# Kernel optimization log

Hardware: AMD Instinct MI355X
Metric: run time of the kernel (lower is better)

## Reference

```python
import jax, jax.numpy as jnp
import numpy as np
import math

PHI = (1 + math.sqrt(5)) / 2
COMPRESS_EXP = 2.0 / 3.0
ALPHA_D = 0.01


def c_mag(z):
    return jnp.sqrt(z[..., 0] ** 2 + z[..., 1] ** 2 + 1e-08)


def c_phase(z):
    return jnp.arctan2(z[..., 1], z[..., 0] + 1e-10)


def c_mul(a, b):
    real = a[..., 0] * b[..., 0] - a[..., 1] * b[..., 1]
    imag = a[..., 0] * b[..., 1] + a[..., 1] * b[..., 0]
    return jnp.stack([real, imag], axis=-1)


@jax.custom_vjp
def fractal_compress(mag):
    return jnp.clip(mag, 1e-08) ** COMPRESS_EXP


def _fc_fwd(mag):
    ms = jnp.clip(mag, 1e-08)
    c = ms ** COMPRESS_EXP
    return c, c / (ms + 1e-06)


def _fc_bwd(ratio, g):
    return (g * jnp.minimum(ratio, 2.0),)


fractal_compress.defvjp(_fc_fwd, _fc_bwd)


def converge(z):
    mag = c_mag(z)
    phase = c_phase(z)
    cm = fractal_compress(mag)
    return jnp.stack([cm * jnp.cos(phase), cm * jnp.sin(phase)], axis=-1)


def setup_inputs():
    key = jax.random.key(0)
    Bsz, T, D, S = 4, 512, 1024, 16
    dt_rank = D // 16
    ks = jax.random.split(key, 8)
    scale = 1.0 / PHI

    def u(k, shape):
        fan_in = shape[1]
        lim = scale / math.sqrt(fan_in)
        return jax.random.uniform(k, shape, minval=-lim, maxval=lim, dtype=jnp.float32)

    return {
        "x": jax.random.normal(ks[0], (Bsz, T, D), dtype=jnp.float32),
        "W_in": u(ks[1], (2 * D, D)),
        "W_xproj": u(ks[2], (dt_rank + 4 * S, D)),
        "W_dt": u(ks[3], (D, dt_rank)),
        "b_dt": jax.random.uniform(ks[4], (D,), minval=-0.1, maxval=0.1, dtype=jnp.float32),
        "W_out": u(ks[5], (D, D)),
        "b_out": jax.random.uniform(ks[6], (D,), minval=-0.1, maxval=0.1, dtype=jnp.float32),
        "W_res": u(ks[7], (2 * S, D)),
        "A_log": jnp.log(jnp.linspace(1.0, float(S), S)),
    }


def reference(x, W_in, W_xproj, W_dt, b_dt, W_out, b_out, W_res, A_log):
    Bsz, T, D = x.shape
    S = A_log.shape[0]
    dt_rank = W_dt.shape[1]

    xz = x @ W_in.T                      # [B,T,2D]
    x_in, z = xz[..., :D], xz[..., D:]
    x_in = jax.nn.silu(x_in)
    xp = x_in @ W_xproj.T                # [B,T,dt_rank+4S]
    dt = jax.nn.softplus(xp[..., :dt_rank] @ W_dt.T + b_dt)   # [B,T,D]
    bc = xp[..., dt_rank:].reshape(Bsz, T, 2, S, 2)
    B_all, C_all = bc[:, :, 0], bc[:, :, 1]                    # [B,T,S,2]

    A_neg = -jnp.exp(A_log)              # [S]

    # initial deep state d: differentiated phases, tiny magnitude
    phases = jnp.linspace(0.0, 2 * math.pi * (1 - 1.0 / S), S)
    d0 = jnp.stack([0.01 * jnp.cos(phases), 0.01 * jnp.sin(phases)], axis=-1)
    d0 = jnp.broadcast_to(d0, (Bsz, S, 2)).astype(x.dtype)
    h0 = jnp.zeros((Bsz, D, S, 2), dtype=x.dtype)

    def step(carry, xs):
        h_prev, d_prev = carry
        x_t, dt_t, B_t, C_t = xs        # [B,D], [B,D], [B,S,2], [B,S,2]
        x_complex = (x_t @ W_res.T).reshape(Bsz, S, 2)
        d_read = jax.lax.stop_gradient(d_prev)
        T_gate = jnp.cos((c_phase(x_complex) - c_phase(d_read)) / 2) ** 2  # [B,S]
        d_mag = c_mag(d_read)[..., None]
        d_normed = d_read / (d_mag + 1e-08)
        d_scale = jnp.sqrt(jnp.clip(d_mag, 1e-06, 20.0))
        surfaced = d_normed * d_scale * T_gate[..., None]                  # [B,S,2]

        alpha = jnp.exp(dt_t[..., None] * A_neg)                           # [B,D,S]
        x_full = jnp.stack([x_t, jnp.zeros_like(x_t)], axis=-1)            # [B,D,2]
        Bx = c_mul(B_t[:, None, :, :], x_full[:, :, None, :])              # [B,D,S,2]
        Bx = Bx + surfaced[:, None, :, :]
        Bx = Bx * dt_t[:, :, None, None]                                   # gamma scaling

        h_decayed = h_prev * alpha[..., None]
        released = h_prev * (1.0 - alpha)[..., None]
        comp = jnp.clip(converge(released), -10.0, 10.0)
        comp_avg = comp.mean(axis=1)                                       # [B,S,2]
        d_t = jax.lax.stop_gradient(d_prev) + ALPHA_D * comp_avg
        d_mag_new = c_mag(d_t)[..., None]
        d_t = jnp.where(d_mag_new > 20.0, d_t * (20.0 / d_mag_new), d_t)

        h_t = h_decayed + Bx
        Ch = c_mul(C_t[:, None, :, :], h_t)                                # [B,D,S,2]
        y_t = Ch[..., 0].sum(axis=-1)                                      # [B,D]
        return (h_t, d_t), y_t

    xs = (
        jnp.swapaxes(x_in, 0, 1),
        jnp.swapaxes(dt, 0, 1),
        jnp.swapaxes(B_all, 0, 1),
        jnp.swapaxes(C_all, 0, 1),
    )
    (_, _), ys = jax.lax.scan(step, (h0, d0), xs)
    y = jnp.swapaxes(ys, 0, 1)           # [B,T,D]
    y = y * jax.nn.silu(z)
    return y @ W_out.T + b_out
```

## Files before the change

### kernel.cpp

```cpp
#include <hip/hip_runtime.h>
#include <hip/hip_bf16.h>
#include <math.h>


enum { EPI_NONE=0, EPI_SILU=1, EPI_SPBIAS=2, EPI_BIAS=3 };

template<int EPI>
__device__ __forceinline__ float epi_apply(float v, float b) {
  if constexpr (EPI == EPI_SILU)        { return v / (1.0f + expf(-v)); }
  else if constexpr (EPI == EPI_SPBIAS) { float t = v + b; return fmaxf(t, 0.0f) + log1pf(expf(-fabsf(t))); }
  else if constexpr (EPI == EPI_BIAS)   { return v + b; }
  else return v;
}

template<int EPI, bool HAS_A2>
__global__ __launch_bounds__(256) void gemm_wt(
    const float* __restrict__ A, int lda,
    const float* __restrict__ A2, int lda2,
    const float* __restrict__ W, int ldw,
    const float* __restrict__ bias,
    float* __restrict__ C, int ldc,
    int N, int K)
{
  constexpr int BM = 64, BN = 64, BK = 32, PAD = 4;
  __shared__ float As[BK][BM + PAD];
  __shared__ float Ws[BK][BN + PAD];
  const int m0 = blockIdx.x * BM;
  const int n0 = blockIdx.y * BN;
  const int tid = threadIdx.x;
  const int tx = tid & 15;
  const int ty = tid >> 4;
  const int lm = tid & 63;
  const int lk = (tid >> 6) << 3;

  float4 a0, a1, w0, w1;
  {
    const float* p = A + (size_t)(m0 + lm) * lda + lk;
    a0 = ((const float4*)p)[0]; a1 = ((const float4*)p)[1];
    if (HAS_A2) {
      const float* p2 = A2 + (size_t)(m0 + lm) * lda2 + lk;
      const float4 b0 = ((const float4*)p2)[0], b1 = ((const float4*)p2)[1];
      a0.x*=b0.x; a0.y*=b0.y; a0.z*=b0.z; a0.w*=b0.w;
      a1.x*=b1.x; a1.y*=b1.y; a1.z*=b1.z; a1.w*=b1.w;
    }
    const int n = n0 + lm;
    if (n < N) {
      const float* pw = W + (size_t)n * ldw + lk;
      w0 = ((const float4*)pw)[0]; w1 = ((const float4*)pw)[1];
    } else { w0 = make_float4(0.f,0.f,0.f,0.f); w1 = w0; }
  }

  float acc[4][4] = {{0.f,0.f,0.f,0.f},{0.f,0.f,0.f,0.f},{0.f,0.f,0.f,0.f},{0.f,0.f,0.f,0.f}};
  const int NT = K / BK;

  for (int i = 0; i < NT; ++i) {
    __syncthreads();
    As[lk+0][lm]=a0.x; As[lk+1][lm]=a0.y; As[lk+2][lm]=a0.z; As[lk+3][lm]=a0.w;
    As[lk+4][lm]=a1.x; As[lk+5][lm]=a1.y; As[lk+6][lm]=a1.z; As[lk+7][lm]=a1.w;
    Ws[lk+0][lm]=w0.x; Ws[lk+1][lm]=w0.y; Ws[lk+2][lm]=w0.z; Ws[lk+3][lm]=w0.w;
    Ws[lk+4][lm]=w1.x; Ws[lk+5][lm]=w1.y; Ws[lk+6][lm]=w1.z; Ws[lk+7][lm]=w1.w;
    __syncthreads();
    if (i + 1 < NT) {
      const int k0 = (i + 1) * BK;
      const float* p = A + (size_t)(m0 + lm) * lda + k0 + lk;
      a0 = ((const float4*)p)[0]; a1 = ((const float4*)p)[1];
      if (HAS_A2) {
        const float* p2 = A2 + (size_t)(m0 + lm) * lda2 + k0 + lk;
        const float4 b0 = ((const float4*)p2)[0], b1 = ((const float4*)p2)[1];
        a0.x*=b0.x; a0.y*=b0.y; a0.z*=b0.z; a0.w*=b0.w;
        a1.x*=b1.x; a1.y*=b1.y; a1.z*=b1.z; a1.w*=b1.w;
      }
      const int n = n0 + lm;
      if (n < N) {
        const float* pw = W + (size_t)n * ldw + k0 + lk;
        w0 = ((const float4*)pw)[0]; w1 = ((const float4*)pw)[1];
      } else { w0 = make_float4(0.f,0.f,0.f,0.f); w1 = w0; }
    }
#pragma unroll
    for (int kk = 0; kk < BK; ++kk) {
      const float4 a = *(const float4*)&As[kk][ty << 2];
      const float4 w = *(const float4*)&Ws[kk][tx << 2];
      const float ar[4] = {a.x, a.y, a.z, a.w};
      const float wr[4] = {w.x, w.y, w.z, w.w};
#pragma unroll
      for (int ii = 0; ii < 4; ++ii)
#pragma unroll
        for (int j = 0; j < 4; ++j)
          acc[ii][j] = fmaf(ar[ii], wr[j], acc[ii][j]);
    }
  }

  const int ncol = n0 + (tx << 2);
  float bj[4] = {0.f, 0.f, 0.f, 0.f};
  if constexpr (EPI == EPI_SPBIAS || EPI == EPI_BIAS) {
    if (ncol < N) { const float4 bv = *(const float4*)(bias + ncol); bj[0]=bv.x; bj[1]=bv.y; bj[2]=bv.z; bj[3]=bv.w; }
  }
  if (ncol < N) {
#pragma unroll
    for (int i = 0; i < 4; ++i) {
      float vs[4];
#pragma unroll
      for (int j = 0; j < 4; ++j) vs[j] = epi_apply<EPI>(acc[i][j], bj[j]);
      *(float4*)(C + (size_t)(m0 + (ty << 2) + i) * ldc + ncol) = make_float4(vs[0], vs[1], vs[2], vs[3]);
    }
  }
}

__global__ __launch_bounds__(256) void gemm_dualw32(
    const float* __restrict__ A, int lda,
    const float* __restrict__ W1,
    const float* __restrict__ W2, int ldw,
    float* __restrict__ C, int ldc, int K)
{
  constexpr int BM = 32, BN = 32, BK = 32, PAD = 4;
  __shared__ float As[BK][BM + PAD];
  __shared__ float Ws[BK][BN + PAD];
  const int m0 = blockIdx.x * BM;
  const int n0 = blockIdx.y * BN;
  const int tid = threadIdx.x;
  const int tx = tid & 15;
  const int ty = tid >> 4;
  const int lm = tid & 31;
  const int lk = (tid >> 5) << 2;

  const int n = n0 + lm;
  const float* wrow = (n < 128) ? (W1 + (size_t)n * ldw) : (W2 + (size_t)(n - 128) * ldw);

  float4 av = *(const float4*)(A + (size_t)(m0 + lm) * lda + lk);
  float4 wv = *(const float4*)(wrow + lk);

  float acc[2][2] = {{0.f,0.f},{0.f,0.f}};
  const int NT = K / BK;
  for (int i = 0; i < NT; ++i) {
    __syncthreads();
    As[lk+0][lm]=av.x; As[lk+1][lm]=av.y; As[lk+2][lm]=av.z; As[lk+3][lm]=av.w;
    Ws[lk+0][lm]=wv.x; Ws[lk+1][lm]=wv.y; Ws[lk+2][lm]=wv.z; Ws[lk+3][lm]=wv.w;
    __syncthreads();
    if (i + 1 < NT) {
      const int k0 = (i + 1) * BK;
      av = *(const float4*)(A + (size_t)(m0 + lm) * lda + k0 + lk);
      wv = *(const float4*)(wrow + k0 + lk);
    }
#pragma unroll
    for (int kk = 0; kk < BK; ++kk) {
      const float2 a = *(const float2*)&As[kk][ty << 1];
      const float2 w = *(const float2*)&Ws[kk][tx << 1];
      acc[0][0] = fmaf(a.x, w.x, acc[0][0]);
      acc[0][1] = fmaf(a.x, w.y, acc[0][1]);
      acc[1][0] = fmaf(a.y, w.x, acc[1][0]);
      acc[1][1] = fmaf(a.y, w.y, acc[1][1]);
    }
  }
  const int ncol = n0 + (tx << 1);
  float* pc = C + (size_t)(m0 + (ty << 1)) * ldc + ncol;
  *(float2*)pc         = make_float2(acc[0][0], acc[0][1]);
  *(float2*)(pc + ldc) = make_float2(acc[1][0], acc[1][1]);
}

__global__ __launch_bounds__(256) void gemm_dt64(
    const float* __restrict__ A, int lda,
    const float* __restrict__ W,
    const float* __restrict__ bias,
    float* __restrict__ C, int ldc)
{
  __shared__ float As[64][68];
  __shared__ float Ws[64][68];
  const int m0 = blockIdx.x * 64;
  const int n0 = blockIdx.y * 64;
  const int tid = threadIdx.x;
  const int lm = tid & 63;
  const int kq = (tid >> 6) << 4;

  {
    const float* pa = A + (size_t)(m0 + lm) * lda + kq;
    const float4 a0 = ((const float4*)pa)[0];
    const float4 a1 = ((const float4*)pa)[1];
    const float4 a2 = ((const float4*)pa)[2];
    const float4 a3 = ((const float4*)pa)[3];
    const float* pw = W + (size_t)(n0 + lm) * 64 + kq;
    const float4 w0 = ((const float4*)pw)[0];
    const float4 w1 = ((const float4*)pw)[1];
    const float4 w2 = ((const float4*)pw)[2];
    const float4 w3 = ((const float4*)pw)[3];
    As[kq+ 0][lm]=a0.x; As[kq+ 1][lm]=a0.y; As[kq+ 2][lm]=a0.z; As[kq+ 3][lm]=a0.w;
    As[kq+ 4][lm]=a1.x; As[kq+ 5][lm]=a1.y; As[kq+ 6][lm]=a1.z; As[kq+ 7][lm]=a1.w;
    As[kq+ 8][lm]=a2.x; As[kq+ 9][lm]=a2.y; As[kq+10][lm]=a2.z; As[kq+11][lm]=a2.w;
    As[kq+12][lm]=a3.x; As[kq+13][lm]=a3.y; As[kq+14][lm]=a3.z; As[kq+15][lm]=a3.w;
    Ws[kq+ 0][lm]=w0.x; Ws[kq+ 1][lm]=w0.y; Ws[kq+ 2][lm]=w0.z; Ws[kq+ 3][lm]=w0.w;
    Ws[kq+ 4][lm]=w1.x; Ws[kq+ 5][lm]=w1.y; Ws[kq+ 6][lm]=w1.z; Ws[kq+ 7][lm]=w1.w;
    Ws[kq+ 8][lm]=w2.x; Ws[kq+ 9][lm]=w2.y; Ws[kq+10][lm]=w2.z; Ws[kq+11][lm]=w2.w;
    Ws[kq+12][lm]=w3.x; Ws[kq+13][lm]=w3.y; Ws[kq+14][lm]=w3.z; Ws[kq+15][lm]=w3.w;
  }
  __syncthreads();

  const int tx = tid & 15;
  const int ty = tid >> 4;
  float acc[4][4] = {{0.f,0.f,0.f,0.f},{0.f,0.f,0.f,0.f},{0.f,0.f,0.f,0.f},{0.f,0.f,0.f,0.f}};
#pragma unroll 16
  for (int kk = 0; kk < 64; ++kk) {
    const float4 a = *(const float4*)&As[kk][ty << 2];
    const float4 w = *(const float4*)&Ws[kk][tx << 2];
    const float ar[4] = {a.x, a.y, a.z, a.w};
    const float wr[4] = {w.x, w.y, w.z, w.w};
#pragma unroll
    for (int i = 0; i < 4; ++i)
#pragma unroll
      for (int j = 0; j < 4; ++j)
        acc[i][j] = fmaf(ar[i], wr[j], acc[i][j]);
  }

  const int ncol = n0 + (tx << 2);
  const float4 bv = *(const float4*)(bias + ncol);
  const float bj[4] = {bv.x, bv.y, bv.z, bv.w};
#pragma unroll
  for (int i = 0; i < 4; ++i) {
    float vs[4];
#pragma unroll
    for (int j = 0; j < 4; ++j) vs[j] = epi_apply<EPI_SPBIAS>(acc[i][j], bj[j]);
    *(float4*)(C + (size_t)(m0 + (ty << 2) + i) * ldc + ncol) = make_float4(vs[0], vs[1], vs[2], vs[3]);
  }
}

__global__ void zero_kernel(float4* __restrict__ p, int n4) {
  const int i = blockIdx.x * blockDim.x + threadIdx.x;
  if (i < n4) p[i] = make_float4(0.f, 0.f, 0.f, 0.f);
}

__global__ __launch_bounds__(256) void reduce_y(const float4* __restrict__ yp, float4* __restrict__ yo, int n4) {
  const int i = blockIdx.x * blockDim.x + threadIdx.x;
  if (i >= n4) return;
  float4 a = yp[i];
#pragma unroll
  for (int s = 1; s < 16; ++s) {
    const float4 v = yp[(size_t)s * 524288 + i];
    a.x += v.x; a.y += v.y; a.z += v.z; a.w += v.w;
  }
  yo[i] = a;
}

template<int CTRL>
__device__ __forceinline__ float dpp_fadd(float x) {
  const int s = __builtin_amdgcn_update_dpp(0, __float_as_int(x), CTRL, 0xF, 0xF, true);
  return x + __int_as_float(s);
}
__device__ __forceinline__ float wave64_sum_l63(float x) {
  x = dpp_fadd<0x111>(x);
  x = dpp_fadd<0x112>(x);
  x = dpp_fadd<0x114>(x);
  x = dpp_fadd<0x118>(x);
  x = dpp_fadd<0x142>(x);
  x = dpp_fadd<0x143>(x);
  return x;
}

__device__ __forceinline__ void comp_block(const float4& dtv, const float na2,
    const float (&h_r)[4], const float (&h_i)[4], float (&al_out)[4],
    float& wr, float& wi)
{
  const float ta[4] = {dtv.x, dtv.y, dtv.z, dtv.w};
  float sr = 0.f, si = 0.f;
#pragma unroll
  for (int e = 0; e < 4; ++e) {
    const float a = exp2f(ta[e] * na2);
    al_out[e] = a;
    const float om    = 1.0f - a;
    const float rel_r = h_r[e] * om, rel_i = h_i[e] * om;
    const float m2 = fmaf(rel_r, rel_r, fmaf(rel_i, rel_i, 1e-8f));
    const float u  = exp2f(log2f(m2) * (-1.0f / 6.0f));
    const float rr = rel_r + 1e-10f;
    float cr = rr * u;    cr = fminf(fmaxf(cr, -10.f), 10.f);
    float ci = rel_i * u; ci = fminf(fmaxf(ci, -10.f), 10.f);
    sr += cr; si += ci;
  }
  wr = wave64_sum_l63(sr);
  wi = wave64_sum_l63(si);
}

template<bool PARTIAL>
__device__ __forceinline__ void step_update(
    float& d_r, float& d_i, const float avg_r, const float avg_i,
    const float2& cx, const float4& xv, const float4& dtv,
    const float2& Bv, const float2& Cv,
    const float (&alv)[4], float (&h_r)[4], float (&h_i)[4],
    float* py)
{
  d_r = fmaf(0.01f, avg_r, d_r);
  d_i = fmaf(0.01f, avg_i, d_i);
  const float dm2c = fmaf(d_r, d_r, fmaf(d_i, d_i, 1e-8f));
  if (dm2c > 400.f) { const float sc = 20.f * __builtin_amdgcn_rsqf(dm2c); d_r *= sc; d_i *= sc; }

  const float xr2 = cx.x + 1e-10f;
  const float irx = __builtin_amdgcn_rsqf(fmaf(xr2, xr2, fmaf(cx.y, cx.y, 1e-38f)));
  const float dr2 = d_r + 1e-10f;
  const float ird = __builtin_amdgcn_rsqf(fmaf(dr2, dr2, fmaf(d_i, d_i, 1e-38f)));
  const float cosdp = fmaf(xr2, dr2, cx.y * d_i) * irx * ird;
  const float Tg  = 0.5f * (1.0f + cosdp);
  const float md2 = fmaf(d_r, d_r, fmaf(d_i, d_i, 1e-8f));
  const float sf  = Tg * exp2f(log2f(md2) * -0.25f);
  const float s_r = d_r * sf, s_i = d_i * sf;

  const float xa[4] = {xv.x, xv.y, xv.z, xv.w};
  const float ta[4] = {dtv.x, dtv.y, dtv.z, dtv.w};
  float yv[4];
#pragma unroll
  for (int e = 0; e < 4; ++e) {
    const float bx_r = fmaf(Bv.x, xa[e], s_r) * ta[e];
    const float bx_i = fmaf(Bv.y, xa[e], s_i) * ta[e];
    h_r[e] = fmaf(h_r[e], alv[e], bx_r);
    h_i[e] = fmaf(h_i[e], alv[e], bx_i);
    yv[e] = fmaf(Cv.x, h_r[e], -(Cv.y * h_i[e]));
  }
  if (PARTIAL) {
    *(float4*)py = make_float4(yv[0], yv[1], yv[2], yv[3]);
  } else {
#pragma unroll
    for (int e = 0; e < 4; ++e) atomicAdd(py + e, yv[e]);
  }
}

template<int RB, int RO, bool PARTIAL>
__device__ __forceinline__ void period_body(
    const float* __restrict__ px, const float* __restrict__ pdt,
    const float* __restrict__ pB, const float* __restrict__ pC,
    const float* __restrict__ pxc, float* __restrict__ py,
    const float na2, const int lane, const int wid,
    float (*red)[4][4],
    float& d_r, float& d_i,
    float (&h_r)[4], float (&h_i)[4], float (&al)[4],
    float4& x0, float4& t0, float2& B0, float2& C0, float2& c0,
    float4& x1, float4& t1, float2& B1, float2& C1, float2& c1,
    const float4& t2)
{
  const float4 qa = *(const float4*)&red[RB][0][0];
  const float4 qb = *(const float4*)&red[RB][1][0];
  const float4 qc = *(const float4*)&red[RB][2][0];
  const float4 qd = *(const float4*)&red[RB][3][0];

  step_update<PARTIAL>(d_r, d_i,
      (qa.x + qb.x + qc.x + qd.x) * (1.0f / 1024.0f),
      (qa.y + qb.y + qc.y + qd.y) * (1.0f / 1024.0f),
      c0, x0, t0, B0, C0, al, h_r, h_i, py + (size_t)RO * 1024);

  x0 = *(const float4*)(px  + (size_t)(RO + 3) * 2048);
  t0 = *(const float4*)(pdt + (size_t)(RO + 3) * 1024);
  B0 = *(const float2*)(pB  + (RO + 3) * 160);
  C0 = *(const float2*)(pC  + (RO + 3) * 160);
  c0 = *(const float2*)(pxc + (RO + 3) * 160);

  float al1[4], w1r, w1i;
  comp_block(t1, na2, h_r, h_i, al1, w1r, w1i);

  step_update<PARTIAL>(d_r, d_i,
      (qa.z + qb.z + qc.z + qd.z) * (1.0f / 1024.0f),
      (qa.w + qb.w + qc.w + qd.w) * (1.0f / 1024.0f),
      c1, x1, t1, B1, C1, al1, h_r, h_i, py + (size_t)(RO + 1) * 1024);

  x1 = *(const float4*)(px  + (size_t)(RO + 4) * 2048);
  t1 = *(const float4*)(pdt + (size_t)(RO + 4) * 1024);
  B1 = *(const float2*)(pB  + (RO + 4) * 160);
  C1 = *(const float2*)(pC  + (RO + 4) * 160);
  c1 = *(const float2*)(pxc + (RO + 4) * 160);

  float w2r, w2i;
  comp_block(t2, na2, h_r, h_i, al, w2r, w2i);

  if (lane == 63) *(float4*)&red[(RB + 1) % 3][wid][0] = make_float4(w1r, w1i, w2r, w2i);

  asm volatile("s_waitcnt lgkmcnt(0)" ::: "memory");
  __builtin_amdgcn_s_barrier();
  asm volatile("" ::: "memory");
}

template<bool PARTIAL>
__global__ __launch_bounds__(256) void scan_g1b(
    const float* __restrict__ xin,
    const float* __restrict__ xpc,
    const float* __restrict__ dtb,
    const float* __restrict__ A_log,
    float* __restrict__ ybase,
    int T,
    const float* __restrict__ xg,
    const float* __restrict__ Wz,
    float* __restrict__ Cz)
{
  if (blockIdx.x < 64) {
    __builtin_amdgcn_s_setprio(1);

    const int b = blockIdx.x >> 4;
    const int s = blockIdx.x & 15;
    const int d0 = threadIdx.x << 2;
    const int lane = threadIdx.x & 63;
    const int wid = threadIdx.x >> 6;

    __shared__ __align__(16) float red[3][4][4];

    const float a_s = expf(A_log[s]);
    const float na2 = -a_s * 1.4426950408889634f;
    const float phase = (float)(6.283185307179586 * (double)s / 16.0);
    float d_r = 0.01f * cosf(phase);
    float d_i = 0.01f * sinf(phase);
    float h_r[4] = {0.f,0.f,0.f,0.f};
    float h_i[4] = {0.f,0.f,0.f,0.f};
    float al[4];

    const size_t rb = (size_t)b * T;
    const float* px  = xin + rb * 2048 + d0;
    const float* pdt = dtb + rb * 1024 + d0;
    const float* pB  = xpc + rb * 160 + 64 + 2 * s;
    const float* pC  = xpc + rb * 160 + 96 + 2 * s;
    const float* pxc = xpc + rb * 160 + 128 + 2 * s;
    float* py = PARTIAL ? (ybase + (size_t)s * (4 * 512 * 1024) + rb * 1024 + d0)
                        : (ybase + rb * 1024 + d0);

    float4 xA = *(const float4*)px;
    float4 tA = *(const float4*)pdt;
    float2 BA = *(const float2*)pB;
    float2 CA = *(const float2*)pC;
    float2 cA = *(const float2*)pxc;
    float4 xB = *(const float4*)(px + 2048);
    float4 tB = *(const float4*)(pdt + 1024);
    float2 BB = *(const float2*)(pB + 160);
    float2 CB = *(const float2*)(pC + 160);
    float2 cB = *(const float2*)(pxc + 160);
    float4 xC = *(const float4*)(px + 2 * 2048);
    float4 tC = *(const float4*)(pdt + 2 * 1024);
    float2 BC = *(const float2*)(pB + 2 * 160);
    float2 CC = *(const float2*)(pC + 2 * 160);
    float2 cC = *(const float2*)(pxc + 2 * 160);

    {
      float w0r, w0i;
      comp_block(tA, na2, h_r, h_i, al, w0r, w0i);
      if (lane == 63) *(float4*)&red[0][wid][0] = make_float4(0.f, 0.f, w0r, w0i);
    }
    __syncthreads();

    for (int it = 0; it < 85; ++it) {
      period_body<0, 0, PARTIAL>(px, pdt, pB, pC, pxc, py, na2, lane, wid, red,
          d_r, d_i, h_r, h_i, al,
          xA, tA, BA, CA, cA,  xB, tB, BB, CB, cB,  tC);
      period_body<1, 2, PARTIAL>(px, pdt, pB, pC, pxc, py, na2, lane, wid, red,
          d_r, d_i, h_r, h_i, al,
          xC, tC, BC, CC, cC,  xA, tA, BA, CA, cA,  tB);
      period_body<2, 4, PARTIAL>(px, pdt, pB, pC, pxc, py, na2, lane, wid, red,
          d_r, d_i, h_r, h_i, al,
          xB, tB, BB, CB, cB,  xC, tC, BC, CC, cC,  tA);
      px += 6 * 2048; pdt += 6 * 1024; pB += 6 * 160; pC += 6 * 160; pxc += 6 * 160;
      py += 6 * 1024;
    }
    period_body<0, 0, PARTIAL>(px, pdt, pB, pC, pxc, py, na2, lane, wid, red,
        d_r, d_i, h_r, h_i, al,
        xA, tA, BA, CA, cA,  xB, tB, BB, CB, cB,  tC);
    __builtin_amdgcn_s_setprio(0);
  } else {
    constexpr int BK = 32, PAD = 4;
    __shared__ float As[BK][64 + PAD];
    __shared__ float Ws[BK][64 + PAD];
    const int b2 = blockIdx.x - 64;
    const int m0 = (b2 & 31) << 6;
    const int n0 = (b2 >> 5) << 6;
    const int tid = threadIdx.x;
    const int tx = tid & 15;
    const int ty = tid >> 4;
    const int lm = tid & 63;
    const int lk = (tid >> 6) << 3;

    float4 a0, a1, w0, w1;
    {
      const float* p = xg + (size_t)(m0 + lm) * 1024 + lk;
      a0 = ((const float4*)p)[0]; a1 = ((const float4*)p)[1];
      const float* pw = Wz + (size_t)(n0 + lm) * 1024 + lk;
      w0 = ((const float4*)pw)[0]; w1 = ((const float4*)pw)[1];
    }
    float acc[4][4] = {{0.f,0.f,0.f,0.f},{0.f,0.f,0.f,0.f},{0.f,0.f,0.f,0.f},{0.f,0.f,0.f,0.f}};
    const int NT = 1024 / BK;
    for (int i = 0; i < NT; ++i) {
      __syncthreads();
      As[lk+0][lm]=a0.x; As[lk+1][lm]=a0.y; As[lk+2][lm]=a0.z; As[lk+3][lm]=a0.w;
      As[lk+4][lm]=a1.x; As[lk+5][lm]=a1.y; As[lk+6][lm]=a1.z; As[lk+7][lm]=a1.w;
      Ws[lk+0][lm]=w0.x; Ws[lk+1][lm]=w0.y; Ws[lk+2][lm]=w0.z; Ws[lk+3][lm]=w0.w;
      Ws[lk+4][lm]=w1.x; Ws[lk+5][lm]=w1.y; Ws[lk+6][lm]=w1.z; Ws[lk+7][lm]=w1.w;
      __syncthreads();
      if (i + 1 < NT) {
        const int k0 = (i + 1) * BK;
        const float* p = xg + (size_t)(m0 + lm) * 1024 + k0 + lk;
        a0 = ((const float4*)p)[0]; a1 = ((const float4*)p)[1];
        const float* pw = Wz + (size_t)(n0 + lm) * 1024 + k0 + lk;
        w0 = ((const float4*)pw)[0]; w1 = ((const float4*)pw)[1];
      }
#pragma unroll
      for (int kk = 0; kk < BK; ++kk) {
        const float4 a = *(const float4*)&As[kk][ty << 2];
        const float4 w = *(const float4*)&Ws[kk][tx << 2];
        const float ar[4] = {a.x, a.y, a.z, a.w};
        const float wr[4] = {w.x, w.y, w.z, w.w};
#pragma unroll
        for (int ii = 0; ii < 4; ++ii)
#pragma unroll
          for (int j = 0; j < 4; ++j)
            acc[ii][j] = fmaf(ar[ii], wr[j], acc[ii][j]);
      }
    }
    const int ncol = n0 + (tx << 2);
#pragma unroll
    for (int i = 0; i < 4; ++i) {
      float vs[4];
#pragma unroll
      for (int j = 0; j < 4; ++j) vs[j] = epi_apply<EPI_SILU>(acc[i][j], 0.f);
      *(float4*)(Cz + (size_t)(m0 + (ty << 2) + i) * 2048 + ncol) = make_float4(vs[0], vs[1], vs[2], vs[3]);
    }
  }
}

extern "C" void kernel_launch(void* const* d_in, const int* in_sizes, int n_in,
                              void* d_out, int out_size, void* d_ws, size_t ws_size,
                              hipStream_t stream) {
  const float* x     = (const float*)d_in[0];
  const float* W_in  = (const float*)d_in[1];
  const float* W_xp  = (const float*)d_in[2];
  const float* W_dt  = (const float*)d_in[3];
  const float* b_dt  = (const float*)d_in[4];
  const float* W_out = (const float*)d_in[5];
  const float* b_out = (const float*)d_in[6];
  const float* W_res = (const float*)d_in[7];
  const float* A_log = (const float*)d_in[8];
  float* out = (float*)d_out;

  float* ws     = (float*)d_ws;
  float* siluxz = ws;
  float* xpc    = siluxz + (size_t)2048 * 2048;
  float* dtb    = xpc    + (size_t)2048 * 160;
  float* ybuf   = dtb    + (size_t)2048 * 1024;
  float* ypart  = ybuf   + (size_t)2048 * 1024;

  const size_t need_bytes = ((size_t)8716288 + (size_t)33554432) * 4;
  const bool use_part = ws_size >= need_bytes;

  gemm_wt<EPI_SILU, false><<<dim3(32, 16), 256, 0, stream>>>(
      x, 1024, nullptr, 0, W_in, 1024, nullptr, siluxz, 2048, 1024, 1024);
  gemm_dualw32<<<dim3(64, 5), 256, 0, stream>>>(
      siluxz, 2048, W_xp, W_res, 1024, xpc, 160, 1024);
  gemm_dt64<<<dim3(32, 16), 256, 0, stream>>>(
      xpc, 160, W_dt, b_dt, dtb, 1024);

  if (use_part) {
    scan_g1b<true><<<dim3(64 + 512), dim3(256), 0, stream>>>(
        siluxz, xpc, dtb, A_log, ypart, 512,
        x, W_in + (size_t)1024 * 1024, siluxz + 1024);
    reduce_y<<<dim3(2048), 256, 0, stream>>>((const float4*)ypart, (float4*)ybuf, 524288);
  } else {
    zero_kernel<<<dim3(2048), 256, 0, stream>>>((float4*)ybuf, (2048 * 1024) / 4);
    scan_g1b<false><<<dim3(64 + 512), dim3(256), 0, stream>>>(
        siluxz, xpc, dtb, A_log, ybuf, 512,
        x, W_in + (size_t)1024 * 1024, siluxz + 1024);
  }

  gemm_wt<EPI_BIAS, true><<<dim3(32, 16), 256, 0, stream>>>(
      ybuf, 1024, siluxz + 1024, 2048, W_out, 1024, b_out, out, 1024, 1024, 1024);
}
```

Before: 495.1 us.

## Replace scan block barriers with LDS counter spin-wait; persistent GEMM side blocks

Inside the scan blocks, each per-period s_barrier becomes a shared-memory atomic counter that the four waves increment and then spin on with a rising target. The goal is to avoid hardware barrier stalls on the serial time loop. The co-scheduled z-GEMM blocks become persistent: 192 blocks loop over the 512 tiles, so the grid shrinks to 256 blocks and every block starts immediately. The spin-waits burn issue slots shared with the co-resident GEMM waves, and the counter uses volatile polling of LDS.

```diff
diff --git a/kernel.cpp b/kernel.cpp
--- a/kernel.cpp
+++ b/kernel.cpp
@@ -324,7 +324,7 @@
     const float* __restrict__ pB, const float* __restrict__ pC,
     const float* __restrict__ pxc, float* __restrict__ py,
     const float na2, const int lane, const int wid,
-    float (*red)[4][4],
+    float (*red)[4][4], int* scnt, int& tgt,
     float& d_r, float& d_i,
     float (&h_r)[4], float (&h_i)[4], float (&al)[4],
     float4& x0, float4& t0, float2& B0, float2& C0, float2& c0,
@@ -367,8 +367,10 @@
   if (lane == 63) *(float4*)&red[(RB + 1) % 3][wid][0] = make_float4(w1r, w1i, w2r, w2i);
 
   asm volatile("s_waitcnt lgkmcnt(0)" ::: "memory");
-  __builtin_amdgcn_s_barrier();
+  if (lane == 63) atomicAdd(scnt, 1);
+  while (*(volatile const int*)scnt < tgt) {}
   asm volatile("" ::: "memory");
+  tgt += 4;
 }
 
 template<bool PARTIAL>
@@ -393,6 +395,8 @@
     const int wid = threadIdx.x >> 6;
 
     __shared__ __align__(16) float red[3][4][4];
+    __shared__ int cnt;
+    if (threadIdx.x == 0) cnt = 0;
 
     const float a_s = expf(A_log[s]);
     const float na2 = -a_s * 1.4426950408889634f;
@@ -428,27 +432,33 @@
     float2 CC = *(const float2*)(pC + 2 * 160);
     float2 cC = *(const float2*)(pxc + 2 * 160);
 
+    __syncthreads();
+
     {
       float w0r, w0i;
       comp_block(tA, na2, h_r, h_i, al, w0r, w0i);
       if (lane == 63) *(float4*)&red[0][wid][0] = make_float4(0.f, 0.f, w0r, w0i);
-    }
-    __syncthreads();
+      asm volatile("s_waitcnt lgkmcnt(0)" ::: "memory");
+      if (lane == 63) atomicAdd(&cnt, 1);
+      while (*(volatile const int*)&cnt < 4) {}
+      asm volatile("" ::: "memory");
+    }
+    int tgt = 8;
 
     for (int it = 0; it < 85; ++it) {
-      period_body<0, 0, PARTIAL>(px, pdt, pB, pC, pxc, py, na2, lane, wid, red,
+      period_body<0, 0, PARTIAL>(px, pdt, pB, pC, pxc, py, na2, lane, wid, red, &cnt, tgt,
           d_r, d_i, h_r, h_i, al,
           xA, tA, BA, CA, cA,  xB, tB, BB, CB, cB,  tC);
-      period_body<1, 2, PARTIAL>(px, pdt, pB, pC, pxc, py, na2, lane, wid, red,
+      period_body<1, 2, PARTIAL>(px, pdt, pB, pC, pxc, py, na2, lane, wid, red, &cnt, tgt,
           d_r, d_i, h_r, h_i, al,
           xC, tC, BC, CC, cC,  xA, tA, BA, CA, cA,  tB);
-      period_body<2, 4, PARTIAL>(px, pdt, pB, pC, pxc, py, na2, lane, wid, red,
+      period_body<2, 4, PARTIAL>(px, pdt, pB, pC, pxc, py, na2, lane, wid, red, &cnt, tgt,
           d_r, d_i, h_r, h_i, al,
           xB, tB, BB, CB, cB,  xC, tC, BC, CC, cC,  tA);
       px += 6 * 2048; pdt += 6 * 1024; pB += 6 * 160; pC += 6 * 160; pxc += 6 * 160;
       py += 6 * 1024;
     }
-    period_body<0, 0, PARTIAL>(px, pdt, pB, pC, pxc, py, na2, lane, wid, red,
+    period_body<0, 0, PARTIAL>(px, pdt, pB, pC, pxc, py, na2, lane, wid, red, &cnt, tgt,
         d_r, d_i, h_r, h_i, al,
         xA, tA, BA, CA, cA,  xB, tB, BB, CB, cB,  tC);
     __builtin_amdgcn_s_setprio(0);
@@ -456,58 +466,62 @@
     constexpr int BK = 32, PAD = 4;
     __shared__ float As[BK][64 + PAD];
     __shared__ float Ws[BK][64 + PAD];
-    const int b2 = blockIdx.x - 64;
-    const int m0 = (b2 & 31) << 6;
-    const int n0 = (b2 >> 5) << 6;
+    const int bg = blockIdx.x - 64;
     const int tid = threadIdx.x;
     const int tx = tid & 15;
     const int ty = tid >> 4;
     const int lm = tid & 63;
     const int lk = (tid >> 6) << 3;
 
-    float4 a0, a1, w0, w1;
-    {
-      const float* p = xg + (size_t)(m0 + lm) * 1024 + lk;
-      a0 = ((const float4*)p)[0]; a1 = ((const float4*)p)[1];
-      const float* pw = Wz + (size_t)(n0 + lm) * 1024 + lk;
-      w0 = ((const float4*)pw)[0]; w1 = ((const float4*)pw)[1];
-    }
-    float acc[4][4] = {{0.f,0.f,0.f,0.f},{0.f,0.f,0.f,0.f},{0.f,0.f,0.f,0.f},{0.f,0.f,0.f,0.f}};
-    const int NT = 1024 / BK;
-    for (int i = 0; i < NT; ++i) {
-      __syncthreads();
-      As[lk+0][lm]=a0.x; As[lk+1][lm]=a0.y; As[lk+2][lm]=a0.z; As[lk+3][lm]=a0.w;
-      As[lk+4][lm]=a1.x; As[lk+5][lm]=a1.y; As[lk+6][lm]=a1.z; As[lk+7][lm]=a1.w;
-      Ws[lk+0][lm]=w0.x; Ws[lk+1][lm]=w0.y; Ws[lk+2][lm]=w0.z; Ws[lk+3][lm]=w0.w;
-      Ws[lk+4][lm]=w1.x; Ws[lk+5][lm]=w1.y; Ws[lk+6][lm]=w1.z; Ws[lk+7][lm]=w1.w;
-      __syncthreads();
-      if (i + 1 < NT) {
-        const int k0 = (i + 1) * BK;
-        const float* p = xg + (size_t)(m0 + lm) * 1024 + k0 + lk;
+    for (int t2 = bg; t2 < 512; t2 += 192) {
+      const int m0 = (t2 & 31) << 6;
+      const int n0 = (t2 >> 5) << 6;
+
+      float4 a0, a1, w0, w1;
+      {
+        const float* p = xg + (size_t)(m0 + lm) * 1024 + lk;
         a0 = ((const float4*)p)[0]; a1 = ((const float4*)p)[1];
-        const float* pw = Wz + (size_t)(n0 + lm) * 1024 + k0 + lk;
+        const float* pw = Wz + (size_t)(n0 + lm) * 1024 + lk;
         w0 = ((const float4*)pw)[0]; w1 = ((const float4*)pw)[1];
       }
-#pragma unroll
-      for (int kk = 0; kk < BK; ++kk) {
-        const float4 a = *(const float4*)&As[kk][ty << 2];
-        const float4 w = *(const float4*)&Ws[kk][tx << 2];
-        const float ar[4] = {a.x, a.y, a.z, a.w};
-        const float wr[4] = {w.x, w.y, w.z, w.w};
-#pragma unroll
-        for (int ii = 0; ii < 4; ++ii)
-#pragma unroll
-          for (int j = 0; j < 4; ++j)
-            acc[ii][j] = fmaf(ar[ii], wr[j], acc[ii][j]);
+      float acc[4][4] = {{0.f,0.f,0.f,0.f},{0.f,0.f,0.f,0.f},{0.f,0.f,0.f,0.f},{0.f,0.f,0.f,0.f}};
+      const int NT = 1024 / BK;
+      for (int i = 0; i < NT; ++i) {
+        __syncthreads();
+        As[lk+0][lm]=a0.x; As[lk+1][lm]=a0.y; As[lk+2][lm]=a0.z; As[lk+3][lm]=a0.w;
+        As[lk+4][lm]=a1.x; As[lk+5][lm]=a1.y; As[lk+6][lm]=a1.z; As[lk+7][lm]=a1.w;
+        Ws[lk+0][lm]=w0.x; Ws[lk+1][lm]=w0.y; Ws[lk+2][lm]=w0.z; Ws[lk+3][lm]=w0.w;
+        Ws[lk+4][lm]=w1.x; Ws[lk+5][lm]=w1.y; Ws[lk+6][lm]=w1.z; Ws[lk+7][lm]=w1.w;
+        __syncthreads();
+        if (i + 1 < NT) {
+          const int k0 = (i + 1) * BK;
+          const float* p = xg + (size_t)(m0 + lm) * 1024 + k0 + lk;
+          a0 = ((const float4*)p)[0]; a1 = ((const float4*)p)[1];
+          const float* pw = Wz + (size_t)(n0 + lm) * 1024 + k0 + lk;
+          w0 = ((const float4*)pw)[0]; w1 = ((const float4*)pw)[1];
+        }
+#pragma unroll
+        for (int kk = 0; kk < BK; ++kk) {
+          const float4 a = *(const float4*)&As[kk][ty << 2];
+          const float4 w = *(const float4*)&Ws[kk][tx << 2];
+          const float ar[4] = {a.x, a.y, a.z, a.w};
+          const float wr[4] = {w.x, w.y, w.z, w.w};
+#pragma unroll
+          for (int ii = 0; ii < 4; ++ii)
+#pragma unroll
+            for (int j = 0; j < 4; ++j)
+              acc[ii][j] = fmaf(ar[ii], wr[j], acc[ii][j]);
+        }
       }
-    }
-    const int ncol = n0 + (tx << 2);
-#pragma unroll
-    for (int i = 0; i < 4; ++i) {
-      float vs[4];
-#pragma unroll
-      for (int j = 0; j < 4; ++j) vs[j] = epi_apply<EPI_SILU>(acc[i][j], 0.f);
-      *(float4*)(Cz + (size_t)(m0 + (ty << 2) + i) * 2048 + ncol) = make_float4(vs[0], vs[1], vs[2], vs[3]);
+      const int ncol = n0 + (tx << 2);
+#pragma unroll
+      for (int i = 0; i < 4; ++i) {
+        float vs[4];
+#pragma unroll
+        for (int j = 0; j < 4; ++j) vs[j] = epi_apply<EPI_SILU>(acc[i][j], 0.f);
+        *(float4*)(Cz + (size_t)(m0 + (ty << 2) + i) * 2048 + ncol) = make_float4(vs[0], vs[1], vs[2], vs[3]);
+      }
+      __syncthreads();
     }
   }
 }
@@ -544,13 +558,13 @@
       xpc, 160, W_dt, b_dt, dtb, 1024);
 
   if (use_part) {
-    scan_g1b<true><<<dim3(64 + 512), dim3(256), 0, stream>>>(
+    scan_g1b<true><<<dim3(256), dim3(256), 0, stream>>>(
         siluxz, xpc, dtb, A_log, ypart, 512,
         x, W_in + (size_t)1024 * 1024, siluxz + 1024);
     reduce_y<<<dim3(2048), 256, 0, stream>>>((const float4*)ypart, (float4*)ybuf, 524288);
   } else {
     zero_kernel<<<dim3(2048), 256, 0, stream>>>((float4*)ybuf, (2048 * 1024) / 4);
-    scan_g1b<false><<<dim3(64 + 512), dim3(256), 0, stream>>>(
+    scan_g1b<false><<<dim3(256), dim3(256), 0, stream>>>(
         siluxz, xpc, dtb, A_log, ybuf, 512,
         x, W_in + (size_t)1024 * 1024, siluxz + 1024);
   }
```

New measurement: 507.9 us. +2.6%, slower.
